# Optimization experiments

Hardware: AMD Instinct MI355X
Metric: run time of the kernel (lower is better)

## Reference

```python
import jax, jax.numpy as jnp
import numpy as np

N_AA = 20          # size of 'ACDEFGHIKLMNPQRSTVWY'
GAP = 20           # gap token; one_hot maps it to an all-zero row (matches '-' skipping)
N_SEQS, SEQ_LEN = 2048, 512
MAX_MI_POS = 100   # min(seq_len, 100) in the source
PSEUDOCOUNT = 0.01


def _features(msa, pc):
    n_seqs, seq_len = msa.shape
    pseudocount = PSEUDOCOUNT * pc[0]

    # one-hot encode; tokens >= N_AA (gaps / unknown) become zero rows,
    # exactly matching the 'if aa in self.aa_to_idx' / "aa != '-'" skips.
    oh = jax.nn.one_hot(msa, N_AA, dtype=jnp.float32)          # [N, L, 20]

    # ---- PSSM ----
    counts = oh.sum(0)                                          # [L, 20]
    freq = (counts + pseudocount) / (n_seqs + pseudocount * N_AA)
    pssm = jnp.log(freq * N_AA + 1e-10)                         # log(freq / (1/20) + 1e-10)

    # ---- Conservation (Shannon entropy over non-gap residues) ----
    total = counts.sum(-1, keepdims=True)                       # [L, 1] non-gap count
    f = counts / jnp.maximum(total, 1.0)
    # f == 0 terms contribute 0 * log2(1e-10) == 0, matching dict-based skipping
    entropy = -(f * jnp.log2(f + 1e-10)).sum(-1)                # [L]
    conservation = jnp.where(total[:, 0] > 0,
                             1.0 - entropy / np.log2(N_AA), 0.0)

    # ---- Mutual information over the first M positions ----
    M = min(seq_len, MAX_MI_POS)
    ohm = oh[:, :M, :]                                          # [N, M, 20]
    # joint counts over sequences where BOTH positions are non-gap
    J = jnp.einsum('nia,njb->ijab', ohm, ohm)                   # [M, M, 20, 20]
    tot = J.sum((2, 3))                                         # [M, M]
    tot_safe = jnp.maximum(tot, 1.0)
    p = J / tot_safe[:, :, None, None]                          # joint prob p_ij
    pi = p.sum(3)[:, :, :, None]                                # marginal p_i (pair-conditioned)
    pj = p.sum(2)[:, :, None, :]                                # marginal p_j
    denom = jnp.maximum(pi * pj, 1e-30)
    term = jnp.where(J > 0, p * jnp.log2(p / denom + 1e-10), 0.0)
    mi = jnp.where(tot > 0, term.sum((2, 3)), 0.0)              # [M, M]
    mi = mi * (1.0 - jnp.eye(M, dtype=mi.dtype))                # diagonal left at 0
    mi_matrix = jnp.zeros((seq_len, seq_len), jnp.float32).at[:M, :M].set(mi)

    return pssm, conservation, mi_matrix


def setup_inputs() -> dict:
    key = jax.random.key(0)
    k1, _ = jax.random.split(key)
    # tokens 0..19 = amino acids, 20 = gap '-'
    msa = jax.random.randint(k1, (N_SEQS, SEQ_LEN), 0, N_AA + 1, dtype=jnp.int32)
    pc = jnp.ones((1,), dtype=jnp.float32)  # pseudocount scale (==1 -> pseudocount 0.01)
    return {"msa": msa, "pc": pc}


def reference(msa, pc):
    return _features(msa, pc)
```

## Files before the change

kernel.cpp:

```cpp
#include <hip/hip_runtime.h>

#define N_SEQS 2048
#define SEQ_LEN 512
#define NAA 20
#define NS 21
#define MPOS 100
#define NPAIRS 4950
#define WPB 4
#define MI_BLOCKS ((NPAIRS + WPB - 1) / WPB)

__global__ __launch_bounds__(256) void pos_kernel(const int* __restrict__ msa,
                                                  const float* __restrict__ pc,
                                                  unsigned char* __restrict__ cols,
                                                  float* __restrict__ pssm,
                                                  float* __restrict__ cons,
                                                  float* __restrict__ mi) {
    __shared__ int hist[4][NS];
    __shared__ int cnt_s[NAA];
    const int i = blockIdx.x;
    const int tid = threadIdx.x;
    const int w = tid >> 6;

    float4* row = (float4*)(mi + (size_t)i * SEQ_LEN);
    if (tid < SEQ_LEN / 4) row[tid] = make_float4(0.f, 0.f, 0.f, 0.f);

    if (tid < 4 * NS) ((int*)hist)[tid] = 0;
    __syncthreads();

    int vals[8];
#pragma unroll
    for (int k = 0; k < 8; ++k) vals[k] = msa[(tid + 256 * k) * SEQ_LEN + i];
    if (i < MPOS) {
#pragma unroll
        for (int k = 0; k < 8; ++k)
            cols[i * N_SEQS + tid + 256 * k] = (unsigned char)vals[k];
    }
#pragma unroll
    for (int k = 0; k < 8; ++k) atomicAdd(&hist[w][vals[k]], 1);
    __syncthreads();

    if (tid < NAA) {
        int c = hist[0][tid] + hist[1][tid] + hist[2][tid] + hist[3][tid];
        cnt_s[tid] = c;
        float pcnt = 0.01f * pc[0];
        float freq = ((float)c + pcnt) / (2048.0f + pcnt * 20.0f);
        pssm[i * NAA + tid] = __logf(freq * 20.0f + 1e-10f);
    }
    __syncthreads();

    if (tid < 64) {
        float fc = (tid < NAA) ? (float)cnt_s[tid] : 0.f;
        float tot = fc;
#pragma unroll
        for (int off = 32; off; off >>= 1) tot += __shfl_xor(tot, off, 64);
        float ts = fmaxf(tot, 1.f);
        float f = __fdividef(fc, ts);
        float term = (tid < NAA) ? -f * __log2f(f + 1e-10f) : 0.f;
#pragma unroll
        for (int off = 32; off; off >>= 1) term += __shfl_xor(term, off, 64);
        if (tid == 0)
            cons[i] = (tot > 0.f) ? (1.f - term * 0.2313782131597592f) : 0.f;
    }
}

__global__ __launch_bounds__(256) void mi_kernel(const unsigned char* __restrict__ cols,
                                                 float* __restrict__ mi) {
    __shared__ int hist[WPB][NS * NS];
    __shared__ float ra_s[WPB][NAA];
    __shared__ float cb_s[WPB][NAA];

    const int tid = threadIdx.x;
    const int w = tid >> 6;
    const int lane = tid & 63;

    int t = blockIdx.x * WPB + w;
    const bool active = (t < NPAIRS);
    if (!active) t = 0;

    int i = (int)((199.0f - sqrtf(39601.0f - 8.0f * (float)t)) * 0.5f);
    if (i < 0) i = 0;
    while ((i + 1) * (198 - i) / 2 <= t) ++i;
    while (i * (199 - i) / 2 > t) --i;
    const int j = i + 1 + (t - i * (199 - i) / 2);

#pragma unroll
    for (int u = 0; u < 7; ++u) {
        int k = lane + 64 * u;
        if (k < NS * NS) hist[w][k] = 0;
    }
    __syncthreads();

    if (active) {
        const uint4* ci = (const uint4*)(cols + i * N_SEQS + lane * 32);
        const uint4* cj = (const uint4*)(cols + j * N_SEQS + lane * 32);
        uint4 A0 = ci[0], A1 = ci[1];
        uint4 B0 = cj[0], B1 = cj[1];
        unsigned int aw[8] = {A0.x, A0.y, A0.z, A0.w, A1.x, A1.y, A1.z, A1.w};
        unsigned int bw[8] = {B0.x, B0.y, B0.z, B0.w, B1.x, B1.y, B1.z, B1.w};
#pragma unroll
        for (int q = 0; q < 8; ++q) {
            unsigned int av = aw[q], bv = bw[q];
#pragma unroll
            for (int byte = 0; byte < 4; ++byte) {
                int a = (av >> (8 * byte)) & 0xFF;
                int b = (bv >> (8 * byte)) & 0xFF;
                atomicAdd(&hist[w][a * NS + b], 1);
            }
        }
    }
    __syncthreads();

    if (lane < NAA) {
        int s = 0;
#pragma unroll
        for (int b = 0; b < NAA; ++b) s += hist[w][lane * NS + b];
        ra_s[w][lane] = (float)s;
    } else if (lane >= 32 && lane < 32 + NAA) {
        int c = lane - 32, s = 0;
#pragma unroll
        for (int a = 0; a < NAA; ++a) s += hist[w][a * NS + c];
        cb_s[w][c] = (float)s;
    }
    __syncthreads();

    float tot = 0.f;
#pragma unroll
    for (int a = 0; a < NAA; ++a) tot += ra_s[w][a];
    const float ts = fmaxf(tot, 1.f);
    const float inv = __fdividef(1.f, ts);

    float part = 0.f;
#pragma unroll
    for (int u = 0; u < 7; ++u) {
        int k = lane + 64 * u;
        if (k < NAA * NAA) {
            int row = k / NAA;
            int col = k - row * NAA;
            int J = hist[w][row * NS + col];
            if (J > 0) {
                float p = (float)J * inv;
                float pi = ra_s[w][row] * inv;
                float pj = cb_s[w][col] * inv;
                float denom = fmaxf(pi * pj, 1e-30f);
                part += p * __log2f(__fdividef(p, denom) + 1e-10f);
            }
        }
    }
#pragma unroll
    for (int off = 32; off; off >>= 1) part += __shfl_down(part, off, 64);

    if (active && lane == 0) {
        float m = (tot > 0.f) ? part : 0.f;
        mi[i * SEQ_LEN + j] = m;
        mi[j * SEQ_LEN + i] = m;
    }
}

extern "C" void kernel_launch(void* const* d_in, const int* in_sizes, int n_in,
                              void* d_out, int out_size, void* d_ws, size_t ws_size,
                              hipStream_t stream) {
    const int* msa = (const int*)d_in[0];
    const float* pc = (const float*)d_in[1];

    float* pssm = (float*)d_out;
    float* cons = pssm + SEQ_LEN * NAA;
    float* mi = cons + SEQ_LEN;

    unsigned char* cols = (unsigned char*)d_ws;

    pos_kernel<<<SEQ_LEN, 256, 0, stream>>>(msa, pc, cols, pssm, cons, mi);
    mi_kernel<<<MI_BLOCKS, 256, 0, stream>>>(cols, mi);
}
```

Baseline: 20.85 us.

## Split coalesced transpose pack from fused per-position and MI kernel

Adds a pack kernel that reads the MSA row-wise with coalesced int4 loads and writes a byte-transposed column array, covering all positions when the workspace is large enough. The per-position statistics work is folded into the MI kernel as extra blocks, so the PSSM/conservation blocks and the pair-histogram blocks run concurrently in one launch. The MI row zeroing no longer touches the first 100 columns of the first 100 rows, and several syncthreads in the per-warp MI path are removed since each warp owns its histogram. The cost is scattered byte writes in the transpose, and a full-size column buffer that depends on the workspace size.

Result: no change. 21.26 us (+2.0%).

```diff
diff --git a/kernel.cpp b/kernel.cpp
--- a/kernel.cpp
+++ b/kernel.cpp
@@ -8,63 +8,38 @@
 #define NPAIRS 4950
 #define WPB 4
 #define MI_BLOCKS ((NPAIRS + WPB - 1) / WPB)
-
-__global__ __launch_bounds__(256) void pos_kernel(const int* __restrict__ msa,
-                                                  const float* __restrict__ pc,
-                                                  unsigned char* __restrict__ cols,
-                                                  float* __restrict__ pssm,
-                                                  float* __restrict__ cons,
-                                                  float* __restrict__ mi) {
-    __shared__ int hist[4][NS];
-    __shared__ int cnt_s[NAA];
-    const int i = blockIdx.x;
+#define K2_GRID (SEQ_LEN + MI_BLOCKS)
+
+__global__ __launch_bounds__(256) void pack_kernel(const int* __restrict__ msa,
+                                                   unsigned char* __restrict__ cols,
+                                                   int full) {
     const int tid = threadIdx.x;
-    const int w = tid >> 6;
-
-    float4* row = (float4*)(mi + (size_t)i * SEQ_LEN);
-    if (tid < SEQ_LEN / 4) row[tid] = make_float4(0.f, 0.f, 0.f, 0.f);
-
-    if (tid < 4 * NS) ((int*)hist)[tid] = 0;
-    __syncthreads();
-
-    int vals[8];
-#pragma unroll
-    for (int k = 0; k < 8; ++k) vals[k] = msa[(tid + 256 * k) * SEQ_LEN + i];
-    if (i < MPOS) {
+    const int r0 = blockIdx.x * 4;
+    const int r = tid >> 6;
+    const int c0 = (tid & 63) * 8;
+    const int row = r0 + r;
+    const int4* src = (const int4*)(msa + (size_t)row * SEQ_LEN + c0);
+    int4 v0 = src[0], v1 = src[1];
+    int v[8] = {v0.x, v0.y, v0.z, v0.w, v1.x, v1.y, v1.z, v1.w};
+    if (full) {
 #pragma unroll
         for (int k = 0; k < 8; ++k)
-            cols[i * N_SEQS + tid + 256 * k] = (unsigned char)vals[k];
-    }
-#pragma unroll
-    for (int k = 0; k < 8; ++k) atomicAdd(&hist[w][vals[k]], 1);
-    __syncthreads();
-
-    if (tid < NAA) {
-        int c = hist[0][tid] + hist[1][tid] + hist[2][tid] + hist[3][tid];
-        cnt_s[tid] = c;
-        float pcnt = 0.01f * pc[0];
-        float freq = ((float)c + pcnt) / (2048.0f + pcnt * 20.0f);
-        pssm[i * NAA + tid] = __logf(freq * 20.0f + 1e-10f);
-    }
-    __syncthreads();
-
-    if (tid < 64) {
-        float fc = (tid < NAA) ? (float)cnt_s[tid] : 0.f;
-        float tot = fc;
-#pragma unroll
-        for (int off = 32; off; off >>= 1) tot += __shfl_xor(tot, off, 64);
-        float ts = fmaxf(tot, 1.f);
-        float f = __fdividef(fc, ts);
-        float term = (tid < NAA) ? -f * __log2f(f + 1e-10f) : 0.f;
-#pragma unroll
-        for (int off = 32; off; off >>= 1) term += __shfl_xor(term, off, 64);
-        if (tid == 0)
-            cons[i] = (tot > 0.f) ? (1.f - term * 0.2313782131597592f) : 0.f;
+            cols[(size_t)(c0 + k) * N_SEQS + row] = (unsigned char)v[k];
+    } else if (c0 < MPOS) {
+#pragma unroll
+        for (int k = 0; k < 8; ++k)
+            if (c0 + k < MPOS)
+                cols[(size_t)(c0 + k) * N_SEQS + row] = (unsigned char)v[k];
     }
 }
 
-__global__ __launch_bounds__(256) void mi_kernel(const unsigned char* __restrict__ cols,
-                                                 float* __restrict__ mi) {
+__global__ __launch_bounds__(256) void main_kernel(const int* __restrict__ msa,
+                                                   const float* __restrict__ pc,
+                                                   const unsigned char* __restrict__ cols,
+                                                   int full,
+                                                   float* __restrict__ pssm,
+                                                   float* __restrict__ cons,
+                                                   float* __restrict__ mi) {
     __shared__ int hist[WPB][NS * NS];
     __shared__ float ra_s[WPB][NAA];
     __shared__ float cb_s[WPB][NAA];
@@ -72,87 +47,140 @@
     const int tid = threadIdx.x;
     const int w = tid >> 6;
     const int lane = tid & 63;
-
-    int t = blockIdx.x * WPB + w;
-    const bool active = (t < NPAIRS);
-    if (!active) t = 0;
-
-    int i = (int)((199.0f - sqrtf(39601.0f - 8.0f * (float)t)) * 0.5f);
-    if (i < 0) i = 0;
-    while ((i + 1) * (198 - i) / 2 <= t) ++i;
-    while (i * (199 - i) / 2 > t) --i;
-    const int j = i + 1 + (t - i * (199 - i) / 2);
-
-#pragma unroll
-    for (int u = 0; u < 7; ++u) {
-        int k = lane + 64 * u;
-        if (k < NS * NS) hist[w][k] = 0;
-    }
-    __syncthreads();
-
-    if (active) {
-        const uint4* ci = (const uint4*)(cols + i * N_SEQS + lane * 32);
-        const uint4* cj = (const uint4*)(cols + j * N_SEQS + lane * 32);
-        uint4 A0 = ci[0], A1 = ci[1];
-        uint4 B0 = cj[0], B1 = cj[1];
-        unsigned int aw[8] = {A0.x, A0.y, A0.z, A0.w, A1.x, A1.y, A1.z, A1.w};
-        unsigned int bw[8] = {B0.x, B0.y, B0.z, B0.w, B1.x, B1.y, B1.z, B1.w};
-#pragma unroll
-        for (int q = 0; q < 8; ++q) {
-            unsigned int av = aw[q], bv = bw[q];
-#pragma unroll
-            for (int byte = 0; byte < 4; ++byte) {
-                int a = (av >> (8 * byte)) & 0xFF;
-                int b = (bv >> (8 * byte)) & 0xFF;
-                atomicAdd(&hist[w][a * NS + b], 1);
+    const int bid = blockIdx.x;
+
+    if (bid < SEQ_LEN) {
+        const int i = bid;
+        float* rowp = mi + (size_t)i * SEQ_LEN;
+        if (i < MPOS) {
+            for (int idx = tid; idx < SEQ_LEN - MPOS; idx += 256)
+                rowp[MPOS + idx] = 0.f;
+            if (tid == 0) rowp[i] = 0.f;
+        } else {
+            if (tid < SEQ_LEN / 4)
+                ((float4*)rowp)[tid] = make_float4(0.f, 0.f, 0.f, 0.f);
+        }
+
+        int* h = hist[w];
+        if (lane < NS) h[lane] = 0;
+
+        int vals[8];
+        if (full) {
+            uint2 dv = *(const uint2*)(cols + (size_t)i * N_SEQS + tid * 8);
+            unsigned long long x = ((unsigned long long)dv.y << 32) | dv.x;
+#pragma unroll
+            for (int k = 0; k < 8; ++k) vals[k] = (int)((x >> (8 * k)) & 0xFF);
+        } else {
+#pragma unroll
+            for (int k = 0; k < 8; ++k)
+                vals[k] = msa[(size_t)(tid + 256 * k) * SEQ_LEN + i];
+        }
+#pragma unroll
+        for (int k = 0; k < 8; ++k) atomicAdd(&h[vals[k]], 1);
+        __syncthreads();
+
+        if (tid < NAA) {
+            int c = hist[0][tid] + hist[1][tid] + hist[2][tid] + hist[3][tid];
+            cb_s[0][tid] = (float)c;
+            float pcnt = 0.01f * pc[0];
+            float freq = ((float)c + pcnt) / (2048.0f + pcnt * 20.0f);
+            pssm[i * NAA + tid] = __logf(freq * 20.0f + 1e-10f);
+        }
+        __syncthreads();
+
+        if (tid < 64) {
+            float fc = (tid < NAA) ? cb_s[0][tid] : 0.f;
+            float tot = fc;
+#pragma unroll
+            for (int off = 32; off; off >>= 1) tot += __shfl_xor(tot, off, 64);
+            float ts = fmaxf(tot, 1.f);
+            float f = __fdividef(fc, ts);
+            float term = (tid < NAA) ? -f * __log2f(f + 1e-10f) : 0.f;
+#pragma unroll
+            for (int off = 32; off; off >>= 1) term += __shfl_xor(term, off, 64);
+            if (tid == 0)
+                cons[i] = (tot > 0.f) ? (1.f - term * 0.2313782131597592f) : 0.f;
+        }
+    } else {
+        int t = (bid - SEQ_LEN) * WPB + w;
+        const bool active = (t < NPAIRS);
+        if (!active) t = 0;
+
+        int i = (int)((199.0f - sqrtf(39601.0f - 8.0f * (float)t)) * 0.5f);
+        if (i < 0) i = 0;
+        while ((i + 1) * (198 - i) / 2 <= t) ++i;
+        while (i * (199 - i) / 2 > t) --i;
+        const int j = i + 1 + (t - i * (199 - i) / 2);
+
+        int* h = hist[w];
+#pragma unroll
+        for (int u = 0; u < 7; ++u) {
+            int k = lane + 64 * u;
+            if (k < NS * NS) h[k] = 0;
+        }
+
+        if (active) {
+            const uint4* ci = (const uint4*)(cols + (size_t)i * N_SEQS + lane * 32);
+            const uint4* cj = (const uint4*)(cols + (size_t)j * N_SEQS + lane * 32);
+            uint4 A0 = ci[0], A1 = ci[1];
+            uint4 B0 = cj[0], B1 = cj[1];
+            unsigned int aw[8] = {A0.x, A0.y, A0.z, A0.w, A1.x, A1.y, A1.z, A1.w};
+            unsigned int bw[8] = {B0.x, B0.y, B0.z, B0.w, B1.x, B1.y, B1.z, B1.w};
+#pragma unroll
+            for (int q = 0; q < 8; ++q) {
+                unsigned int av = aw[q], bv = bw[q];
+#pragma unroll
+                for (int byte = 0; byte < 4; ++byte) {
+                    int a = (av >> (8 * byte)) & 0xFF;
+                    int b = (bv >> (8 * byte)) & 0xFF;
+                    atomicAdd(&h[a * NS + b], 1);
+                }
             }
         }
-    }
-    __syncthreads();
-
-    if (lane < NAA) {
-        int s = 0;
-#pragma unroll
-        for (int b = 0; b < NAA; ++b) s += hist[w][lane * NS + b];
-        ra_s[w][lane] = (float)s;
-    } else if (lane >= 32 && lane < 32 + NAA) {
-        int c = lane - 32, s = 0;
-#pragma unroll
-        for (int a = 0; a < NAA; ++a) s += hist[w][a * NS + c];
-        cb_s[w][c] = (float)s;
-    }
-    __syncthreads();
-
-    float tot = 0.f;
-#pragma unroll
-    for (int a = 0; a < NAA; ++a) tot += ra_s[w][a];
-    const float ts = fmaxf(tot, 1.f);
-    const float inv = __fdividef(1.f, ts);
-
-    float part = 0.f;
-#pragma unroll
-    for (int u = 0; u < 7; ++u) {
-        int k = lane + 64 * u;
-        if (k < NAA * NAA) {
-            int row = k / NAA;
-            int col = k - row * NAA;
-            int J = hist[w][row * NS + col];
-            if (J > 0) {
-                float p = (float)J * inv;
-                float pi = ra_s[w][row] * inv;
-                float pj = cb_s[w][col] * inv;
-                float denom = fmaxf(pi * pj, 1e-30f);
-                part += p * __log2f(__fdividef(p, denom) + 1e-10f);
+
+        if (lane < NAA) {
+            int s = 0;
+#pragma unroll
+            for (int b = 0; b < NAA; ++b) s += h[lane * NS + b];
+            ra_s[w][lane] = (float)s;
+        } else if (lane >= 32 && lane < 32 + NAA) {
+            int c = lane - 32, s = 0;
+#pragma unroll
+            for (int a = 0; a < NAA; ++a) s += h[a * NS + c];
+            cb_s[w][c] = (float)s;
+        }
+
+        float tot = 0.f;
+#pragma unroll
+        for (int a = 0; a < NAA; ++a) tot += ra_s[w][a];
+        const float ts = fmaxf(tot, 1.f);
+        const float inv = __fdividef(1.f, ts);
+
+        float part = 0.f;
+#pragma unroll
+        for (int u = 0; u < 7; ++u) {
+            int k = lane + 64 * u;
+            if (k < NAA * NAA) {
+                int row = k / NAA;
+                int col = k - row * NAA;
+                int J = h[row * NS + col];
+                if (J > 0) {
+                    float p = (float)J * inv;
+                    float pi = ra_s[w][row] * inv;
+                    float pj = cb_s[w][col] * inv;
+                    float denom = fmaxf(pi * pj, 1e-30f);
+                    part += p * __log2f(__fdividef(p, denom) + 1e-10f);
+                }
             }
         }
-    }
-#pragma unroll
-    for (int off = 32; off; off >>= 1) part += __shfl_down(part, off, 64);
-
-    if (active && lane == 0) {
-        float m = (tot > 0.f) ? part : 0.f;
-        mi[i * SEQ_LEN + j] = m;
-        mi[j * SEQ_LEN + i] = m;
+#pragma unroll
+        for (int off = 32; off; off >>= 1) part += __shfl_down(part, off, 64);
+
+        if (active && lane == 0) {
+            float m = (tot > 0.f) ? part : 0.f;
+            mi[(size_t)i * SEQ_LEN + j] = m;
+            mi[(size_t)j * SEQ_LEN + i] = m;
+        }
     }
 }
 
@@ -167,7 +195,8 @@
     float* mi = cons + SEQ_LEN;
 
     unsigned char* cols = (unsigned char*)d_ws;
-
-    pos_kernel<<<SEQ_LEN, 256, 0, stream>>>(msa, pc, cols, pssm, cons, mi);
-    mi_kernel<<<MI_BLOCKS, 256, 0, stream>>>(cols, mi);
+    const int full = (ws_size >= (size_t)SEQ_LEN * N_SEQS) ? 1 : 0;
+
+    pack_kernel<<<SEQ_LEN, 256, 0, stream>>>(msa, cols, full);
+    main_kernel<<<K2_GRID, 256, 0, stream>>>(msa, pc, cols, full, pssm, cons, mi);
 }
```

## Fuse position stats and MI into one kernel with 4x4 pair tiles

Applied to the files above, without the earlier changes.

Merges the two kernels into a single launch. Blocks either compute MI for a 4x4 tile of position pairs, reading int4 vectors straight from the MSA with 16 shared histograms, or compute PSSM and conservation for 8 positions plus zeroing of the MI matrix. This drops the second launch, the byte-column workspace round trip and the per-pair reloads of columns. The trade-offs are heavier shared memory per block (16 histograms), redundant lower-triangle work on diagonal tiles, and strided int4 reads across the MSA rows.

Measured after the change: 19.64 us. 1.06x faster.

```diff
diff --git a/kernel.cpp b/kernel.cpp
--- a/kernel.cpp
+++ b/kernel.cpp
@@ -5,154 +5,174 @@
 #define NAA 20
 #define NS 21
 #define MPOS 100
-#define NPAIRS 4950
-#define WPB 4
-#define MI_BLOCKS ((NPAIRS + WPB - 1) / WPB)
+#define G 4
+#define NG (MPOS / G)
+#define NTILE (NG * (NG + 1) / 2)
+#define POSB (SEQ_LEN / 8)
+#define HBINS (NS * NS)
 
-__global__ __launch_bounds__(256) void pos_kernel(const int* __restrict__ msa,
-                                                  const float* __restrict__ pc,
-                                                  unsigned char* __restrict__ cols,
-                                                  float* __restrict__ pssm,
-                                                  float* __restrict__ cons,
-                                                  float* __restrict__ mi) {
-    __shared__ int hist[4][NS];
-    __shared__ int cnt_s[NAA];
-    const int i = blockIdx.x;
-    const int tid = threadIdx.x;
-    const int w = tid >> 6;
-
-    float4* row = (float4*)(mi + (size_t)i * SEQ_LEN);
-    if (tid < SEQ_LEN / 4) row[tid] = make_float4(0.f, 0.f, 0.f, 0.f);
-
-    if (tid < 4 * NS) ((int*)hist)[tid] = 0;
-    __syncthreads();
-
-    int vals[8];
-#pragma unroll
-    for (int k = 0; k < 8; ++k) vals[k] = msa[(tid + 256 * k) * SEQ_LEN + i];
-    if (i < MPOS) {
-#pragma unroll
-        for (int k = 0; k < 8; ++k)
-            cols[i * N_SEQS + tid + 256 * k] = (unsigned char)vals[k];
-    }
-#pragma unroll
-    for (int k = 0; k < 8; ++k) atomicAdd(&hist[w][vals[k]], 1);
-    __syncthreads();
-
-    if (tid < NAA) {
-        int c = hist[0][tid] + hist[1][tid] + hist[2][tid] + hist[3][tid];
-        cnt_s[tid] = c;
-        float pcnt = 0.01f * pc[0];
-        float freq = ((float)c + pcnt) / (2048.0f + pcnt * 20.0f);
-        pssm[i * NAA + tid] = __logf(freq * 20.0f + 1e-10f);
-    }
-    __syncthreads();
-
-    if (tid < 64) {
-        float fc = (tid < NAA) ? (float)cnt_s[tid] : 0.f;
-        float tot = fc;
-#pragma unroll
-        for (int off = 32; off; off >>= 1) tot += __shfl_xor(tot, off, 64);
-        float ts = fmaxf(tot, 1.f);
-        float f = __fdividef(fc, ts);
-        float term = (tid < NAA) ? -f * __log2f(f + 1e-10f) : 0.f;
-#pragma unroll
-        for (int off = 32; off; off >>= 1) term += __shfl_xor(term, off, 64);
-        if (tid == 0)
-            cons[i] = (tot > 0.f) ? (1.f - term * 0.2313782131597592f) : 0.f;
-    }
-}
-
-__global__ __launch_bounds__(256) void mi_kernel(const unsigned char* __restrict__ cols,
-                                                 float* __restrict__ mi) {
-    __shared__ int hist[WPB][NS * NS];
-    __shared__ float ra_s[WPB][NAA];
-    __shared__ float cb_s[WPB][NAA];
+__global__ __launch_bounds__(256) void fused_kernel(const int* __restrict__ msa,
+                                                    const float* __restrict__ pc,
+                                                    float* __restrict__ pssm,
+                                                    float* __restrict__ cons,
+                                                    float* __restrict__ mi) {
+    __shared__ int h_s[16 * HBINS];
+    __shared__ float ra_s[4][NAA], cb_s[4][NAA];
 
     const int tid = threadIdx.x;
     const int w = tid >> 6;
     const int lane = tid & 63;
+    const int bid = blockIdx.x;
 
-    int t = blockIdx.x * WPB + w;
-    const bool active = (t < NPAIRS);
-    if (!active) t = 0;
+    if (bid < NTILE) {
+        int t = bid, ti = 0, off = 0;
+        while (off + (NG - ti) <= t) { off += NG - ti; ++ti; }
+        const int tj = ti + (t - off);
+        const int i0 = ti * G, j0 = tj * G;
+        const bool diag = (ti == tj);
 
-    int i = (int)((199.0f - sqrtf(39601.0f - 8.0f * (float)t)) * 0.5f);
-    if (i < 0) i = 0;
-    while ((i + 1) * (198 - i) / 2 <= t) ++i;
-    while (i * (199 - i) / 2 > t) --i;
-    const int j = i + 1 + (t - i * (199 - i) / 2);
+        for (int k = tid; k < 16 * HBINS; k += 256) h_s[k] = 0;
+        __syncthreads();
 
 #pragma unroll
-    for (int u = 0; u < 7; ++u) {
-        int k = lane + 64 * u;
-        if (k < NS * NS) hist[w][k] = 0;
-    }
-    __syncthreads();
+        for (int k = 0; k < 8; ++k) {
+            const int s = tid + (k << 8);
+            const int* rp = msa + (size_t)s * SEQ_LEN;
+            const int4 va = *(const int4*)(rp + i0);
+            const int4 vb = *(const int4*)(rp + j0);
+            const int A0 = va.x * 21, A1 = va.y * 21, A2 = va.z * 21, A3 = va.w * 21;
+            const int B0 = vb.x, B1 = vb.y, B2 = vb.z, B3 = vb.w;
+            atomicAdd(&h_s[0 * 1764 + 0 * 441 + A0 + B0], 1);
+            atomicAdd(&h_s[0 * 1764 + 1 * 441 + A0 + B1], 1);
+            atomicAdd(&h_s[0 * 1764 + 2 * 441 + A0 + B2], 1);
+            atomicAdd(&h_s[0 * 1764 + 3 * 441 + A0 + B3], 1);
+            atomicAdd(&h_s[1 * 1764 + 0 * 441 + A1 + B0], 1);
+            atomicAdd(&h_s[1 * 1764 + 1 * 441 + A1 + B1], 1);
+            atomicAdd(&h_s[1 * 1764 + 2 * 441 + A1 + B2], 1);
+            atomicAdd(&h_s[1 * 1764 + 3 * 441 + A1 + B3], 1);
+            atomicAdd(&h_s[2 * 1764 + 0 * 441 + A2 + B0], 1);
+            atomicAdd(&h_s[2 * 1764 + 1 * 441 + A2 + B1], 1);
+            atomicAdd(&h_s[2 * 1764 + 2 * 441 + A2 + B2], 1);
+            atomicAdd(&h_s[2 * 1764 + 3 * 441 + A2 + B3], 1);
+            atomicAdd(&h_s[3 * 1764 + 0 * 441 + A3 + B0], 1);
+            atomicAdd(&h_s[3 * 1764 + 1 * 441 + A3 + B1], 1);
+            atomicAdd(&h_s[3 * 1764 + 2 * 441 + A3 + B2], 1);
+            atomicAdd(&h_s[3 * 1764 + 3 * 441 + A3 + B3], 1);
+        }
+        __syncthreads();
 
-    if (active) {
-        const uint4* ci = (const uint4*)(cols + i * N_SEQS + lane * 32);
-        const uint4* cj = (const uint4*)(cols + j * N_SEQS + lane * 32);
-        uint4 A0 = ci[0], A1 = ci[1];
-        uint4 B0 = cj[0], B1 = cj[1];
-        unsigned int aw[8] = {A0.x, A0.y, A0.z, A0.w, A1.x, A1.y, A1.z, A1.w};
-        unsigned int bw[8] = {B0.x, B0.y, B0.z, B0.w, B1.x, B1.y, B1.z, B1.w};
 #pragma unroll
-        for (int q = 0; q < 8; ++q) {
-            unsigned int av = aw[q], bv = bw[q];
+        for (int q = 0; q < 4; ++q) {
+            const int p = w * 4 + q;
+            const int pi = p >> 2, pj = p & 3;
+            if (diag && pi >= pj) continue;
+            const int* h = h_s + p * HBINS;
+
+            if (lane < NAA) {
+                int s = 0;
 #pragma unroll
-            for (int byte = 0; byte < 4; ++byte) {
-                int a = (av >> (8 * byte)) & 0xFF;
-                int b = (bv >> (8 * byte)) & 0xFF;
-                atomicAdd(&hist[w][a * NS + b], 1);
+                for (int b = 0; b < NAA; ++b) s += h[lane * NS + b];
+                ra_s[w][lane] = (float)s;
+            } else if (lane >= 32 && lane < 32 + NAA) {
+                int c = lane - 32, s = 0;
+#pragma unroll
+                for (int a = 0; a < NAA; ++a) s += h[a * NS + c];
+                cb_s[w][c] = (float)s;
+            }
+
+            float tot = 0.f;
+#pragma unroll
+            for (int a = 0; a < NAA; ++a) tot += ra_s[w][a];
+            const float ts = fmaxf(tot, 1.f);
+            const float inv = __fdividef(1.f, ts);
+
+            float part = 0.f;
+#pragma unroll
+            for (int u = 0; u < 7; ++u) {
+                const int k = lane + 64 * u;
+                if (k < NAA * NAA) {
+                    const int row = k / NAA;
+                    const int col = k - row * NAA;
+                    const int J = h[row * NS + col];
+                    if (J > 0) {
+                        float pp = (float)J * inv;
+                        float pi_f = ra_s[w][row] * inv;
+                        float pj_f = cb_s[w][col] * inv;
+                        float denom = fmaxf(pi_f * pj_f, 1e-30f);
+                        part += pp * __log2f(__fdividef(pp, denom) + 1e-10f);
+                    }
+                }
+            }
+#pragma unroll
+            for (int o = 32; o; o >>= 1) part += __shfl_down(part, o, 64);
+
+            if (lane == 0) {
+                const float m = (tot > 0.f) ? part : 0.f;
+                mi[(size_t)(i0 + pi) * SEQ_LEN + (j0 + pj)] = m;
+                mi[(size_t)(j0 + pj) * SEQ_LEN + (i0 + pi)] = m;
             }
         }
-    }
-    __syncthreads();
+    } else {
+        const int pb = bid - NTILE;
+        const int i0 = pb * 8;
 
-    if (lane < NAA) {
-        int s = 0;
-#pragma unroll
-        for (int b = 0; b < NAA; ++b) s += hist[w][lane * NS + b];
-        ra_s[w][lane] = (float)s;
-    } else if (lane >= 32 && lane < 32 + NAA) {
-        int c = lane - 32, s = 0;
-#pragma unroll
-        for (int a = 0; a < NAA; ++a) s += hist[w][a * NS + c];
-        cb_s[w][c] = (float)s;
-    }
-    __syncthreads();
-
-    float tot = 0.f;
-#pragma unroll
-    for (int a = 0; a < NAA; ++a) tot += ra_s[w][a];
-    const float ts = fmaxf(tot, 1.f);
-    const float inv = __fdividef(1.f, ts);
-
-    float part = 0.f;
-#pragma unroll
-    for (int u = 0; u < 7; ++u) {
-        int k = lane + 64 * u;
-        if (k < NAA * NAA) {
-            int row = k / NAA;
-            int col = k - row * NAA;
-            int J = hist[w][row * NS + col];
-            if (J > 0) {
-                float p = (float)J * inv;
-                float pi = ra_s[w][row] * inv;
-                float pj = cb_s[w][col] * inv;
-                float denom = fmaxf(pi * pj, 1e-30f);
-                part += p * __log2f(__fdividef(p, denom) + 1e-10f);
+        for (int r = 0; r < 8; ++r) {
+            const int i = i0 + r;
+            float* rowp = mi + (size_t)i * SEQ_LEN;
+            if (i < MPOS) {
+                for (int c = MPOS + tid; c < SEQ_LEN; c += 256) rowp[c] = 0.f;
+                if (tid == 0) rowp[i] = 0.f;
+            } else {
+                if (tid < SEQ_LEN / 4)
+                    ((float4*)rowp)[tid] = make_float4(0.f, 0.f, 0.f, 0.f);
             }
         }
-    }
+
+        for (int k = tid; k < 4 * 8 * NS; k += 256) h_s[k] = 0;
+        __syncthreads();
+
+        int* h = h_s + w * (8 * NS);
 #pragma unroll
-    for (int off = 32; off; off >>= 1) part += __shfl_down(part, off, 64);
+        for (int k = 0; k < 8; ++k) {
+            const int s = tid + (k << 8);
+            const int* rp = msa + (size_t)s * SEQ_LEN + i0;
+            const int4 v0 = *(const int4*)rp;
+            const int4 v1 = *(const int4*)(rp + 4);
+            atomicAdd(&h[0 * NS + v0.x], 1);
+            atomicAdd(&h[1 * NS + v0.y], 1);
+            atomicAdd(&h[2 * NS + v0.z], 1);
+            atomicAdd(&h[3 * NS + v0.w], 1);
+            atomicAdd(&h[4 * NS + v1.x], 1);
+            atomicAdd(&h[5 * NS + v1.y], 1);
+            atomicAdd(&h[6 * NS + v1.z], 1);
+            atomicAdd(&h[7 * NS + v1.w], 1);
+        }
+        __syncthreads();
 
-    if (active && lane == 0) {
-        float m = (tot > 0.f) ? part : 0.f;
-        mi[i * SEQ_LEN + j] = m;
-        mi[j * SEQ_LEN + i] = m;
+        float* cntf = (float*)(h_s + 1024);
+        if (tid < 8 * NAA) {
+            const int p = tid / NAA, a = tid - p * NAA;
+            const int idx = p * NS + a;
+            const int c = h_s[idx] + h_s[168 + idx] + h_s[336 + idx] + h_s[504 + idx];
+            cntf[tid] = (float)c;
+            const float pcnt = 0.01f * pc[0];
+            const float freq = __fdividef((float)c + pcnt, 2048.0f + pcnt * 20.0f);
+            pssm[(size_t)(i0 + p) * NAA + a] = __logf(freq * 20.0f + 1e-10f);
+        }
+        __syncthreads();
+
+        const int p = tid >> 5, l = tid & 31;
+        const float fc = (l < NAA) ? cntf[p * NAA + l] : 0.f;
+        float tt = fc;
+#pragma unroll
+        for (int o = 16; o; o >>= 1) tt += __shfl_xor(tt, o, 32);
+        const float ts2 = fmaxf(tt, 1.f);
+        const float f = __fdividef(fc, ts2);
+        float term = (l < NAA) ? -f * __log2f(f + 1e-10f) : 0.f;
+#pragma unroll
+        for (int o = 16; o; o >>= 1) term += __shfl_xor(term, o, 32);
+        if (l == 0)
+            cons[i0 + p] = (tt > 0.f) ? (1.f - term * 0.2313782131597592f) : 0.f;
     }
 }
 
@@ -166,8 +186,5 @@
     float* cons = pssm + SEQ_LEN * NAA;
     float* mi = cons + SEQ_LEN;
 
-    unsigned char* cols = (unsigned char*)d_ws;
-
-    pos_kernel<<<SEQ_LEN, 256, 0, stream>>>(msa, pc, cols, pssm, cons, mi);
-    mi_kernel<<<MI_BLOCKS, 256, 0, stream>>>(cols, mi);
+    fused_kernel<<<NTILE + POSB, 256, 0, stream>>>(msa, pc, pssm, cons, mi);
 }
```
